# Optimization experiments

Measured on AMD Instinct MI355X. Metric: run time of the kernel, lower is better.

## Reference

```python
import jax, jax.numpy as jnp
import numpy as np

C = 128        # channels
NHEADS = 8
B = 16
HW = 128       # image side; must satisfy HW*HW == C**2 for the module's final view


def setup_inputs() -> dict:
    key = jax.random.key(0)
    k0, k1, k2, k3, k4 = jax.random.split(key, 5)
    x = jax.random.normal(k0, (B, C, HW, HW), jnp.float32)
    w_qkv = jax.random.normal(k1, (3 * C, C), jnp.float32) * 0.02  # 1x1 conv == dense over channel dim
    b_qkv = jax.random.normal(k2, (3 * C,), jnp.float32) * 0.02
    w_out = jax.random.normal(k3, (C, C), jnp.float32) * 0.02
    b_out = jax.random.normal(k4, (C,), jnp.float32) * 0.02
    return {"x": x, "w_qkv": w_qkv, "b_qkv": b_qkv, "w_out": w_out, "b_out": b_out}


def reference(x, w_qkv, b_qkv, w_out, b_out):
    Bx, Cx, Hs, Ws = x.shape
    d = Cx // NHEADS
    N = Hs * Ws  # flattened spatial tokens
    # QKV 1x1 conv (bias=True)
    qkv = jnp.einsum('oc,bchw->bohw', w_qkv, x) + b_qkv[None, :, None, None]
    q, k, v = jnp.split(qkv, 3, axis=1)          # each (B, C, H, W)
    q = q.reshape(Bx, NHEADS, d, N)
    k = k.reshape(Bx, NHEADS, d, N)
    v = v.reshape(Bx, NHEADS, d, N)
    # scaled dot-product attention over the head-channel dim (d x d scores)
    scores = jnp.einsum('bhdn,bhen->bhde', q, k) / jnp.sqrt(jnp.float32(Cx))
    attn = jax.nn.softmax(scores, axis=-1)
    out = jnp.einsum('bhde,bhen->bhdn', attn, v)  # (B, H, d, N)
    side = N // Cx  # module reshapes to (B, C, N//C, N//C); valid since N == C^2
    out = out.reshape(Bx, Cx, side, side)
    # output 1x1 conv
    return jnp.einsum('oc,bchw->bohw', w_out, out) + b_out[None, :, None, None]
```

## Files before the change

kernel.cpp:

```cpp
#include <hip/hip_runtime.h>
#include <math.h>

#define BB 16
#define CC 128
#define NN 16384
#define NHEADS 8
#define HD 16
#define SCALE 0.08838834764831843f

typedef __attribute__((ext_vector_type(8))) short short8;
typedef __attribute__((ext_vector_type(4))) unsigned short ushort4v;
typedef __attribute__((ext_vector_type(16))) float f32x16;

#define CVT(comp, hh, ll)                                                    \
    {                                                                        \
        unsigned int u = __float_as_uint(comp);                              \
        hh = (unsigned short)(u >> 16);                                      \
        float lf = (comp) - __uint_as_float(u & 0xffff0000u);                \
        ll = (unsigned short)(__float_as_uint(lf) >> 16);                    \
    }

__global__ __launch_bounds__(512, 4) void k1_gram(const float* __restrict__ x,
                                                  float* __restrict__ pG,
                                                  float* __restrict__ pS,
                                                  int CH) {
    const int chunk = blockIdx.x;
    const int b = blockIdx.y;
    const int tid = threadIdx.x;
    const int w = tid >> 6;
    const int l = tid & 63;
    const int lr = l & 31, lh = l >> 5;
    const int ch0 = tid >> 4;
    const int t4 = tid & 15;
    const int NCB = NN / CH;
    const int NSTAGE = NCB >> 6;

    __shared__ __align__(16) unsigned short lds[2][2][128 * 64];

    const float* xg = x + (size_t)b * CC * NN + (size_t)chunk * NCB;

    const int bi = w >> 1;
    const int bj0 = (w & 1) * 2;

    f32x16 a0, a1;
#pragma unroll
    for (int r = 0; r < 16; ++r) { a0[r] = 0.0f; a1[r] = 0.0f; }

    float csum[4] = {0.0f, 0.0f, 0.0f, 0.0f};
    float4 ld[4];

    auto LOAD = [&](int s) {
#pragma unroll
        for (int k = 0; k < 4; ++k)
            ld[k] = *(const float4*)(xg + (size_t)(ch0 + 32 * k) * NN + s * 64 + t4 * 4);
    };

    auto CVW = [&](int buf) {
#pragma unroll
        for (int k = 0; k < 4; ++k) {
            float4 v = ld[k];
            csum[k] += v.x + v.y + v.z + v.w;
            const int ch = ch0 + 32 * k;
            const int idx = ((ch << 6) + (t4 << 2)) ^ ((ch & 7) << 3);
            unsigned short h0, h1, h2, h3, l0, l1, l2, l3;
            CVT(v.x, h0, l0)
            CVT(v.y, h1, l1)
            CVT(v.z, h2, l2)
            CVT(v.w, h3, l3)
            ushort4v hv = {h0, h1, h2, h3};
            ushort4v lv = {l0, l1, l2, l3};
            *(ushort4v*)&lds[buf][0][idx] = hv;
            *(ushort4v*)&lds[buf][1][idx] = lv;
        }
    };

    LOAD(0);
    CVW(0);
    __syncthreads();

    const int chA = bi * 32 + lr;
    const int chB0 = bj0 * 32 + lr;
    const int chB1 = chB0 + 32;
    const int swz = (lr & 7) << 3;

    for (int s = 0; s < NSTAGE; ++s) {
        const int bsel = s & 1;
        if (s + 1 < NSTAGE) LOAD(s + 1);

#pragma unroll
        for (int ks = 0; ks < 4; ++ks) {
            const int tok = ks * 16 + 8 * lh;
            const int idxA = ((chA << 6) + tok) ^ swz;
            const int idxB0 = ((chB0 << 6) + tok) ^ swz;
            const int idxB1 = ((chB1 << 6) + tok) ^ swz;
            short8 ah = *(const short8*)&lds[bsel][0][idxA];
            short8 al = *(const short8*)&lds[bsel][1][idxA];
            short8 b0h = *(const short8*)&lds[bsel][0][idxB0];
            short8 b0l = *(const short8*)&lds[bsel][1][idxB0];
            short8 b1h = *(const short8*)&lds[bsel][0][idxB1];
            short8 b1l = *(const short8*)&lds[bsel][1][idxB1];
            a0 = __builtin_amdgcn_mfma_f32_32x32x16_bf16(ah, b0h, a0, 0, 0, 0);
            a0 = __builtin_amdgcn_mfma_f32_32x32x16_bf16(ah, b0l, a0, 0, 0, 0);
            a0 = __builtin_amdgcn_mfma_f32_32x32x16_bf16(al, b0h, a0, 0, 0, 0);
            a1 = __builtin_amdgcn_mfma_f32_32x32x16_bf16(ah, b1h, a1, 0, 0, 0);
            a1 = __builtin_amdgcn_mfma_f32_32x32x16_bf16(ah, b1l, a1, 0, 0, 0);
            a1 = __builtin_amdgcn_mfma_f32_32x32x16_bf16(al, b1h, a1, 0, 0, 0);
        }

        if (s + 1 < NSTAGE) CVW((s + 1) & 1);
        __syncthreads();
    }

    float* scr = (float*)&lds[0][0][0];
#pragma unroll
    for (int k = 0; k < 4; ++k) scr[(ch0 + 32 * k) * 16 + t4] = csum[k];
    __syncthreads();
    if (tid < 128) {
        float s2 = 0.0f;
#pragma unroll
        for (int i = 0; i < 16; ++i) s2 += scr[tid * 16 + i];
        pS[(size_t)(b * CH + chunk) * 128 + tid] = s2;
    }

    float* outp = pG + (size_t)(b * CH + chunk) * 16384;
#pragma unroll
    for (int r = 0; r < 16; ++r) {
        outp[(2 * w) * 1024 + r * 64 + l] = a0[r];
        outp[(2 * w + 1) * 1024 + r * 64 + l] = a1[r];
    }
}

__global__ __launch_bounds__(256) void k1_reduce(const float* __restrict__ pG,
                                                 const float* __restrict__ pS,
                                                 float* __restrict__ G,
                                                 float* __restrict__ sB,
                                                 int CH) {
    const int sg = blockIdx.x;
    const int b = blockIdx.y;
    const int tid = threadIdx.x;

    if (sg < 64) {
        const int e = sg * 256 + tid;
        const int t = e >> 10;
        const int rl = e & 1023;
        float sum = 0.0f;
        const float* p = pG + (size_t)b * CH * 16384 + e;
        for (int ch = 0; ch < CH; ++ch) sum += p[(size_t)ch * 16384];

        const int bi = t >> 2, bj = t & 3;
        const int reg = rl >> 6, lane = rl & 63;
        const int col = bj * 32 + (lane & 31);
        const int row = bi * 32 + (reg & 3) + 8 * (reg >> 2) + 4 * (lane >> 5);
        G[((size_t)b << 14) + row * CC + col] = sum;
    } else {
        if (tid < 128) {
            float s2 = 0.0f;
            for (int ch = 0; ch < CH; ++ch) s2 += pS[(size_t)(b * CH + ch) * 128 + tid];
            sB[b * CC + tid] = s2;
        }
    }
}

__global__ __launch_bounds__(256) void k2a_attn(const float* __restrict__ G,
                                                const float* __restrict__ sB,
                                                const float* __restrict__ w_qkv,
                                                const float* __restrict__ b_qkv,
                                                float* __restrict__ attn,
                                                float* __restrict__ cpre) {
    const int h = blockIdx.x;
    const int b = blockIdx.y;
    const int tid = threadIdx.x;

    __shared__ float Gs[CC * CC];
    __shared__ float wq_s[HD][132], wk_s[HD][132], Tq[HD][132];
    __shared__ float qs[HD], ks[HD], bqv[HD], bkv[HD], bvv[HD];
    __shared__ float sc[HD][HD + 1];

    {
        const float4* Gv = (const float4*)(G + ((size_t)b << 14));
        float4* Gsv = (float4*)Gs;
#pragma unroll
        for (int i = 0; i < 16; ++i) Gsv[tid + 256 * i] = Gv[tid + 256 * i];
    }
    for (int idx = tid; idx < HD * CC; idx += 256) {
        int r = idx >> 7, c = idx & 127;
        wq_s[r][c] = w_qkv[(h * HD + r) * CC + c];
        wk_s[r][c] = w_qkv[(CC + h * HD + r) * CC + c];
    }
    if (tid < HD) {
        bqv[tid] = b_qkv[h * HD + tid];
        bkv[tid] = b_qkv[CC + h * HD + tid];
        bvv[tid] = b_qkv[2 * CC + h * HD + tid];
    }
    __syncthreads();

    if (tid < 32) {
        int i = tid & 15;
        bool isK = tid >= 16;
        float sum = 0.0f;
        for (int c = 0; c < CC; ++c)
            sum += (isK ? wk_s[i][c] : wq_s[i][c]) * sB[b * CC + c];
        if (isK) ks[i] = sum; else qs[i] = sum;
    }

    {
        const int c2 = tid & 127;
        const int dh = tid >> 7;
        float t[8];
#pragma unroll
        for (int j = 0; j < 8; ++j) t[j] = 0.0f;
        for (int c1 = 0; c1 < CC; ++c1) {
            float g = Gs[c1 * CC + c2];
#pragma unroll
            for (int j = 0; j < 8; ++j) t[j] += wq_s[dh * 8 + j][c1] * g;
        }
        __syncthreads();
#pragma unroll
        for (int j = 0; j < 8; ++j) Tq[dh * 8 + j][c2] = t[j];
    }
    __syncthreads();

    {
        const int dd = tid >> 4, e = tid & 15;
        float sum = 0.0f;
        for (int c2 = 0; c2 < CC; ++c2) sum += Tq[dd][c2] * wk_s[e][c2];
        sum += qs[dd] * bkv[e] + bqv[dd] * ks[e] + (float)NN * bqv[dd] * bkv[e];
        sc[dd][e] = sum * SCALE;
    }
    __syncthreads();

    if (tid < HD) {
        const int dd = tid;
        float mx = -1e30f;
#pragma unroll
        for (int e = 0; e < HD; ++e) mx = fmaxf(mx, sc[dd][e]);
        float ex[HD];
        float den = 0.0f;
#pragma unroll
        for (int e = 0; e < HD; ++e) { ex[e] = __expf(sc[dd][e] - mx); den += ex[e]; }
        float inv = 1.0f / den;
        float cp = 0.0f;
#pragma unroll
        for (int e = 0; e < HD; ++e) {
            float a = ex[e] * inv;
            attn[((size_t)b * NHEADS + h) * HD * HD + dd * HD + e] = a;
            cp += a * bvv[e];
        }
        cpre[b * CC + h * HD + dd] = cp;
    }
}

__global__ __launch_bounds__(256) void k2b_M(const float* __restrict__ attn,
                                             const float* __restrict__ cpre,
                                             const float* __restrict__ w_qkv,
                                             const float* __restrict__ w_out,
                                             const float* __restrict__ b_out,
                                             unsigned short* __restrict__ Mh,
                                             unsigned short* __restrict__ Ml,
                                             float* __restrict__ cvec) {
    const int og = blockIdx.x;
    const int b = blockIdx.y;
    const int tid = threadIdx.x;

    __shared__ float Ph[HD][132];
    __shared__ float Vs[HD][132];
    __shared__ float wo_s[32][129];
    __shared__ float attn_s[CC][HD];
    __shared__ float cpre_s[CC];

    for (int idx = tid; idx < CC * HD; idx += 256)
        attn_s[idx >> 4][idx & 15] = attn[(size_t)b * CC * HD + idx];
    for (int idx = tid; idx < 32 * CC; idx += 256)
        wo_s[idx >> 7][idx & 127] = w_out[(og * 32 + (idx >> 7)) * CC + (idx & 127)];
    if (tid < CC) cpre_s[tid] = cpre[b * CC + tid];
    __syncthreads();

    const int c = tid & 127;
    const int oh = tid >> 7;
    float m[16];
#pragma unroll
    for (int j = 0; j < 16; ++j) m[j] = 0.0f;

    for (int hh = 0; hh < NHEADS; ++hh) {
        for (int idx = tid; idx < HD * CC; idx += 256)
            Vs[idx >> 7][idx & 127] = w_qkv[(2 * CC + hh * HD + (idx >> 7)) * CC + (idx & 127)];
        __syncthreads();
        for (int idx = tid; idx < HD * CC; idx += 256) {
            int dd = idx >> 7, cc = idx & 127;
            float s = 0.0f;
#pragma unroll
            for (int e = 0; e < HD; ++e)
                s += attn_s[hh * HD + dd][e] * Vs[e][cc];
            Ph[dd][cc] = s;
        }
        __syncthreads();
#pragma unroll
        for (int dd = 0; dd < HD; ++dd) {
            float p = Ph[dd][c];
#pragma unroll
            for (int j = 0; j < 16; ++j)
                m[j] += wo_s[oh * 16 + j][hh * HD + dd] * p;
        }
        __syncthreads();
    }

#pragma unroll
    for (int j = 0; j < 16; ++j) {
        const int o = og * 32 + oh * 16 + j;
        unsigned short hh2, ll2;
        CVT(m[j], hh2, ll2)
        Mh[((size_t)b << 14) + o * CC + c] = hh2;
        Ml[((size_t)b << 14) + o * CC + c] = ll2;
    }

    if (tid < 32) {
        float s = 0.0f;
        for (int r = 0; r < CC; ++r) s += wo_s[tid][r] * cpre_s[r];
        cvec[b * CC + og * 32 + tid] = s + b_out[og * 32 + tid];
    }
}

__global__ __launch_bounds__(256, 4) void k3_out(const float* __restrict__ x,
                                                 const unsigned short* __restrict__ Mh,
                                                 const unsigned short* __restrict__ Ml,
                                                 const float* __restrict__ cvec,
                                                 float* __restrict__ y) {
    const int chunk = blockIdx.x;
    const int b = blockIdx.y;
    const int tid = threadIdx.x;
    const int w = tid >> 6;
    const int lane = tid & 63;

    __shared__ __align__(16) unsigned short xs[2][2][64 * 128];

    const float* xb = x + (size_t)b * CC * NN + (size_t)chunk * 256;

    short8 Ah[8], Al[8];
    {
        const size_t mbase = ((size_t)b << 14) + (size_t)(32 * w + (lane & 31)) * CC;
#pragma unroll
        for (int ks = 0; ks < 8; ++ks) {
            const size_t off = mbase + 16 * ks + 8 * (lane >> 5);
            Ah[ks] = *(const short8*)&Mh[off];
            Al[ks] = *(const short8*)&Ml[off];
        }
    }

    float cvv[16];
#pragma unroll
    for (int r = 0; r < 16; ++r)
        cvv[r] = cvec[b * CC + 32 * w + (r & 3) + 8 * (r >> 2) + 4 * (lane >> 5)];

    float ldv[4][4];

    auto LOADH = [&](int s, int hf) {
#pragma unroll
        for (int k = 0; k < 4; ++k) {
            const int c0 = w * 4 + (4 * hf + k) * 16;
#pragma unroll
            for (int i = 0; i < 4; ++i)
                ldv[k][i] = xb[(size_t)(c0 + i) * NN + s * 64 + lane];
        }
    };

    auto CVWH = [&](int buf, int hf) {
#pragma unroll
        for (int k = 0; k < 4; ++k) {
            const int c0 = w * 4 + (4 * hf + k) * 16;
            const int idx = lane * 128 + (c0 ^ ((lane & 7) << 3));
            ushort4v hv, lv;
#pragma unroll
            for (int i = 0; i < 4; ++i) {
                unsigned short hh, ll;
                CVT(ldv[k][i], hh, ll)
                hv[i] = hh;
                lv[i] = ll;
            }
            *(ushort4v*)&xs[buf][0][idx] = hv;
            *(ushort4v*)&xs[buf][1][idx] = lv;
        }
    };

    LOADH(0, 0); CVWH(0, 0);
    LOADH(0, 1); CVWH(0, 1);
    __syncthreads();

    float* yb = y + (size_t)b * CC * NN + (size_t)chunk * 256;
    const int nl0 = lane & 31;
    const int cx0 = (nl0 & 7) << 3;
    const int nl1 = 32 + nl0;

    for (int s = 0; s < 4; ++s) {
        const int bsel = s & 1;
        f32x16 a0, a1;
#pragma unroll
        for (int r = 0; r < 16; ++r) { a0[r] = 0.0f; a1[r] = 0.0f; }

        if (s < 3) LOADH(s + 1, 0);

#pragma unroll
        for (int ks = 0; ks < 8; ++ks) {
            const int idx = nl0 * 128 + ((16 * ks + 8 * (lane >> 5)) ^ cx0);
            short8 bh = *(const short8*)&xs[bsel][0][idx];
            short8 bl = *(const short8*)&xs[bsel][1][idx];
            a0 = __builtin_amdgcn_mfma_f32_32x32x16_bf16(Ah[ks], bh, a0, 0, 0, 0);
            a0 = __builtin_amdgcn_mfma_f32_32x32x16_bf16(Ah[ks], bl, a0, 0, 0, 0);
            a0 = __builtin_amdgcn_mfma_f32_32x32x16_bf16(Al[ks], bh, a0, 0, 0, 0);
        }

        if (s < 3) { CVWH(bsel ^ 1, 0); LOADH(s + 1, 1); }

#pragma unroll
        for (int ks = 0; ks < 8; ++ks) {
            const int idx = nl1 * 128 + ((16 * ks + 8 * (lane >> 5)) ^ cx0);
            short8 bh = *(const short8*)&xs[bsel][0][idx];
            short8 bl = *(const short8*)&xs[bsel][1][idx];
            a1 = __builtin_amdgcn_mfma_f32_32x32x16_bf16(Ah[ks], bh, a1, 0, 0, 0);
            a1 = __builtin_amdgcn_mfma_f32_32x32x16_bf16(Ah[ks], bl, a1, 0, 0, 0);
            a1 = __builtin_amdgcn_mfma_f32_32x32x16_bf16(Al[ks], bh, a1, 0, 0, 0);
        }

        if (s < 3) CVWH(bsel ^ 1, 1);

#pragma unroll
        for (int r = 0; r < 16; ++r) {
            const int o = 32 * w + (r & 3) + 8 * (r >> 2) + 4 * (lane >> 5);
            yb[(size_t)o * NN + s * 64 + nl0] = a0[r] + cvv[r];
            yb[(size_t)o * NN + s * 64 + nl1] = a1[r] + cvv[r];
        }
        __syncthreads();
    }
}

extern "C" void kernel_launch(void* const* d_in, const int* in_sizes, int n_in,
                              void* d_out, int out_size, void* d_ws, size_t ws_size,
                              hipStream_t stream) {
    const float* x     = (const float*)d_in[0];
    const float* w_qkv = (const float*)d_in[1];
    const float* b_qkv = (const float*)d_in[2];
    const float* w_out = (const float*)d_in[3];
    const float* b_out = (const float*)d_in[4];
    float* y = (float*)d_out;

    const size_t szG = (size_t)BB * CC * CC;
    const size_t szS = (size_t)BB * CC;
    const size_t szAttn = (size_t)BB * NHEADS * HD * HD;
    const size_t tail = szG + szS + szAttn + szS + szG + szS;

    int CH = 32;
    while (CH > 1 &&
           ((size_t)CH * BB * 16384 + (size_t)CH * BB * CC + tail) * sizeof(float) > ws_size)
        CH >>= 1;

    float* pG   = (float*)d_ws;
    float* pS   = pG + (size_t)CH * BB * 16384;
    float* G    = pS + (size_t)CH * BB * CC;
    float* sB   = G + szG;
    float* attn = sB + szS;
    float* cpre = attn + szAttn;
    float* Mslab = cpre + szS;
    float* cvec = Mslab + szG;

    unsigned short* Mh = (unsigned short*)Mslab;
    unsigned short* Ml = Mh + (size_t)BB * CC * CC;

    k1_gram<<<dim3(CH, BB), 512, 0, stream>>>(x, pG, pS, CH);
    k1_reduce<<<dim3(65, BB), 256, 0, stream>>>(pG, pS, G, sB, CH);
    k2a_attn<<<dim3(NHEADS, BB), 256, 0, stream>>>(G, sB, w_qkv, b_qkv, attn, cpre);
    k2b_M<<<dim3(4, BB), 256, 0, stream>>>(attn, cpre, w_qkv, w_out, b_out, Mh, Ml, cvec);
    k3_out<<<dim3(64, BB), 256, 0, stream>>>(x, Mh, Ml, cvec, y);
}
```

Before: 348.0 us.

## Shrink LDS tiles and restructure Gram and output kernels for higher occupancy

The Gram kernel drops to 256 threads with 32-token stages and a single LDS buffer, and each wave now computes four 32x32 output tiles. The chunk count doubles to 64. The output kernel uses 32-token stages with a single-buffered LDS tile and reads the bias from shared memory. Both kernels raise wave priority around their MFMA loops. The goal is lower LDS footprint and more resident blocks for this memory-bound pipeline, at the cost of an extra barrier per stage, less load/compute overlap, and a larger partial-Gram workspace to reduce.

```diff
diff --git a/kernel.cpp b/kernel.cpp
--- a/kernel.cpp
+++ b/kernel.cpp
@@ -20,7 +20,7 @@
         ll = (unsigned short)(__float_as_uint(lf) >> 16);                    \
     }
 
-__global__ __launch_bounds__(512, 4) void k1_gram(const float* __restrict__ x,
+__global__ __launch_bounds__(256, 4) void k1_gram(const float* __restrict__ x,
                                                   float* __restrict__ pG,
                                                   float* __restrict__ pS,
                                                   int CH) {
@@ -30,104 +30,109 @@
     const int w = tid >> 6;
     const int l = tid & 63;
     const int lr = l & 31, lh = l >> 5;
-    const int ch0 = tid >> 4;
-    const int t4 = tid & 15;
+    const int ch0 = tid >> 3;
+    const int t4 = tid & 7;
     const int NCB = NN / CH;
-    const int NSTAGE = NCB >> 6;
-
-    __shared__ __align__(16) unsigned short lds[2][2][128 * 64];
+    const int NSTAGE = NCB >> 5;
+
+    __shared__ __align__(16) unsigned short lds[2][64 * 64];
+    __shared__ float scr[128 * 8];
 
     const float* xg = x + (size_t)b * CC * NN + (size_t)chunk * NCB;
 
-    const int bi = w >> 1;
-    const int bj0 = (w & 1) * 2;
-
-    f32x16 a0, a1;
-#pragma unroll
-    for (int r = 0; r < 16; ++r) { a0[r] = 0.0f; a1[r] = 0.0f; }
+    f32x16 acc[4];
+#pragma unroll
+    for (int t = 0; t < 4; ++t)
+#pragma unroll
+        for (int r = 0; r < 16; ++r) acc[t][r] = 0.0f;
 
     float csum[4] = {0.0f, 0.0f, 0.0f, 0.0f};
     float4 ld[4];
+    ushort4v hv[4], lv[4];
 
     auto LOAD = [&](int s) {
 #pragma unroll
         for (int k = 0; k < 4; ++k)
-            ld[k] = *(const float4*)(xg + (size_t)(ch0 + 32 * k) * NN + s * 64 + t4 * 4);
-    };
-
-    auto CVW = [&](int buf) {
+            ld[k] = *(const float4*)(xg + (size_t)(ch0 + 32 * k) * NN + s * 32 + t4 * 4);
+    };
+
+    auto CVTALL = [&]() {
 #pragma unroll
         for (int k = 0; k < 4; ++k) {
             float4 v = ld[k];
             csum[k] += v.x + v.y + v.z + v.w;
-            const int ch = ch0 + 32 * k;
-            const int idx = ((ch << 6) + (t4 << 2)) ^ ((ch & 7) << 3);
             unsigned short h0, h1, h2, h3, l0, l1, l2, l3;
             CVT(v.x, h0, l0)
             CVT(v.y, h1, l1)
             CVT(v.z, h2, l2)
             CVT(v.w, h3, l3)
-            ushort4v hv = {h0, h1, h2, h3};
-            ushort4v lv = {l0, l1, l2, l3};
-            *(ushort4v*)&lds[buf][0][idx] = hv;
-            *(ushort4v*)&lds[buf][1][idx] = lv;
+            hv[k] = ushort4v{h0, h1, h2, h3};
+            lv[k] = ushort4v{l0, l1, l2, l3};
+        }
+    };
+
+    auto WR = [&]() {
+#pragma unroll
+        for (int k = 0; k < 4; ++k) {
+            const int ch = ch0 + 32 * k;
+            const int col = ((ch >> 6) * 32 + t4 * 4) ^ ((ch & 7) << 3);
+            const int idx = (ch & 63) * 64 + col;
+            *(ushort4v*)&lds[0][idx] = hv[k];
+            *(ushort4v*)&lds[1][idx] = lv[k];
         }
     };
 
     LOAD(0);
-    CVW(0);
-    __syncthreads();
-
-    const int chA = bi * 32 + lr;
-    const int chB0 = bj0 * 32 + lr;
-    const int chB1 = chB0 + 32;
-    const int swz = (lr & 7) << 3;
+    CVTALL();
+    WR();
+    __syncthreads();
 
     for (int s = 0; s < NSTAGE; ++s) {
-        const int bsel = s & 1;
         if (s + 1 < NSTAGE) LOAD(s + 1);
 
-#pragma unroll
-        for (int ks = 0; ks < 4; ++ks) {
-            const int tok = ks * 16 + 8 * lh;
-            const int idxA = ((chA << 6) + tok) ^ swz;
-            const int idxB0 = ((chB0 << 6) + tok) ^ swz;
-            const int idxB1 = ((chB1 << 6) + tok) ^ swz;
-            short8 ah = *(const short8*)&lds[bsel][0][idxA];
-            short8 al = *(const short8*)&lds[bsel][1][idxA];
-            short8 b0h = *(const short8*)&lds[bsel][0][idxB0];
-            short8 b0l = *(const short8*)&lds[bsel][1][idxB0];
-            short8 b1h = *(const short8*)&lds[bsel][0][idxB1];
-            short8 b1l = *(const short8*)&lds[bsel][1][idxB1];
-            a0 = __builtin_amdgcn_mfma_f32_32x32x16_bf16(ah, b0h, a0, 0, 0, 0);
-            a0 = __builtin_amdgcn_mfma_f32_32x32x16_bf16(ah, b0l, a0, 0, 0, 0);
-            a0 = __builtin_amdgcn_mfma_f32_32x32x16_bf16(al, b0h, a0, 0, 0, 0);
-            a1 = __builtin_amdgcn_mfma_f32_32x32x16_bf16(ah, b1h, a1, 0, 0, 0);
-            a1 = __builtin_amdgcn_mfma_f32_32x32x16_bf16(ah, b1l, a1, 0, 0, 0);
-            a1 = __builtin_amdgcn_mfma_f32_32x32x16_bf16(al, b1h, a1, 0, 0, 0);
-        }
-
-        if (s + 1 < NSTAGE) CVW((s + 1) & 1);
-        __syncthreads();
-    }
-
-    float* scr = (float*)&lds[0][0][0];
-#pragma unroll
-    for (int k = 0; k < 4; ++k) scr[(ch0 + 32 * k) * 16 + t4] = csum[k];
+        __builtin_amdgcn_s_setprio(1);
+#pragma unroll
+        for (int ks = 0; ks < 2; ++ks) {
+            const int tb = ks * 16 + 8 * lh;
+            const int chA = 32 * w + lr;
+            const int idxA = (chA & 63) * 64 + ((((chA >> 6) * 32) + tb) ^ ((chA & 7) << 3));
+            short8 ah = *(const short8*)&lds[0][idxA];
+            short8 al = *(const short8*)&lds[1][idxA];
+#pragma unroll
+            for (int bj = 0; bj < 4; ++bj) {
+                const int chB = 32 * bj + lr;
+                const int idxB = (chB & 63) * 64 + ((((chB >> 6) * 32) + tb) ^ ((chB & 7) << 3));
+                short8 bh = *(const short8*)&lds[0][idxB];
+                short8 bl = *(const short8*)&lds[1][idxB];
+                acc[bj] = __builtin_amdgcn_mfma_f32_32x32x16_bf16(ah, bh, acc[bj], 0, 0, 0);
+                acc[bj] = __builtin_amdgcn_mfma_f32_32x32x16_bf16(ah, bl, acc[bj], 0, 0, 0);
+                acc[bj] = __builtin_amdgcn_mfma_f32_32x32x16_bf16(al, bh, acc[bj], 0, 0, 0);
+            }
+        }
+        __builtin_amdgcn_s_setprio(0);
+
+        if (s + 1 < NSTAGE) CVTALL();
+        __syncthreads();
+        if (s + 1 < NSTAGE) WR();
+        __syncthreads();
+    }
+
+#pragma unroll
+    for (int k = 0; k < 4; ++k) scr[(ch0 + 32 * k) * 8 + t4] = csum[k];
     __syncthreads();
     if (tid < 128) {
         float s2 = 0.0f;
 #pragma unroll
-        for (int i = 0; i < 16; ++i) s2 += scr[tid * 16 + i];
+        for (int i = 0; i < 8; ++i) s2 += scr[tid * 8 + i];
         pS[(size_t)(b * CH + chunk) * 128 + tid] = s2;
     }
 
     float* outp = pG + (size_t)(b * CH + chunk) * 16384;
 #pragma unroll
-    for (int r = 0; r < 16; ++r) {
-        outp[(2 * w) * 1024 + r * 64 + l] = a0[r];
-        outp[(2 * w + 1) * 1024 + r * 64 + l] = a1[r];
-    }
+    for (int bj = 0; bj < 4; ++bj)
+#pragma unroll
+        for (int r = 0; r < 16; ++r)
+            outp[(4 * w + bj) * 1024 + r * 64 + l] = acc[bj][r];
 }
 
 __global__ __launch_bounds__(256) void k1_reduce(const float* __restrict__ pG,
@@ -330,10 +335,15 @@
     const int tid = threadIdx.x;
     const int w = tid >> 6;
     const int lane = tid & 63;
-
-    __shared__ __align__(16) unsigned short xs[2][2][64 * 128];
+    const int st = tid & 31;
+    const int sc0 = (tid >> 5) * 16;
+
+    __shared__ __align__(16) unsigned short xs[2][32 * 128];
+    __shared__ float csl[CC];
 
     const float* xb = x + (size_t)b * CC * NN + (size_t)chunk * 256;
+
+    if (tid < CC) csl[tid] = cvec[b * CC + tid];
 
     short8 Ah[8], Al[8];
     {
@@ -346,88 +356,77 @@
         }
     }
 
-    float cvv[16];
-#pragma unroll
-    for (int r = 0; r < 16; ++r)
-        cvv[r] = cvec[b * CC + 32 * w + (r & 3) + 8 * (r >> 2) + 4 * (lane >> 5)];
-
-    float ldv[4][4];
-
-    auto LOADH = [&](int s, int hf) {
-#pragma unroll
-        for (int k = 0; k < 4; ++k) {
-            const int c0 = w * 4 + (4 * hf + k) * 16;
-#pragma unroll
-            for (int i = 0; i < 4; ++i)
-                ldv[k][i] = xb[(size_t)(c0 + i) * NN + s * 64 + lane];
-        }
-    };
-
-    auto CVWH = [&](int buf, int hf) {
-#pragma unroll
-        for (int k = 0; k < 4; ++k) {
-            const int c0 = w * 4 + (4 * hf + k) * 16;
-            const int idx = lane * 128 + (c0 ^ ((lane & 7) << 3));
-            ushort4v hv, lv;
-#pragma unroll
-            for (int i = 0; i < 4; ++i) {
-                unsigned short hh, ll;
-                CVT(ldv[k][i], hh, ll)
-                hv[i] = hh;
-                lv[i] = ll;
-            }
-            *(ushort4v*)&xs[buf][0][idx] = hv;
-            *(ushort4v*)&xs[buf][1][idx] = lv;
-        }
-    };
-
-    LOADH(0, 0); CVWH(0, 0);
-    LOADH(0, 1); CVWH(0, 1);
+    float ldv[16];
+    ushort4v hv[4], lv[4];
+
+    auto LOAD = [&](int s) {
+#pragma unroll
+        for (int i = 0; i < 16; ++i)
+            ldv[i] = xb[(size_t)(sc0 + i) * NN + s * 32 + st];
+    };
+
+    auto CVTALL = [&]() {
+#pragma unroll
+        for (int g = 0; g < 4; ++g) {
+            unsigned short h0, h1, h2, h3, l0, l1, l2, l3;
+            CVT(ldv[4 * g + 0], h0, l0)
+            CVT(ldv[4 * g + 1], h1, l1)
+            CVT(ldv[4 * g + 2], h2, l2)
+            CVT(ldv[4 * g + 3], h3, l3)
+            hv[g] = ushort4v{h0, h1, h2, h3};
+            lv[g] = ushort4v{l0, l1, l2, l3};
+        }
+    };
+
+    auto WR = [&]() {
+        const int v = (st & 7) << 3;
+        const int rowb = st * 128;
+#pragma unroll
+        for (int g = 0; g < 4; ++g) {
+            const int idx = rowb + ((sc0 + 4 * g) ^ v);
+            *(ushort4v*)&xs[0][idx] = hv[g];
+            *(ushort4v*)&xs[1][idx] = lv[g];
+        }
+    };
+
+    LOAD(0);
+    CVTALL();
+    WR();
     __syncthreads();
 
     float* yb = y + (size_t)b * CC * NN + (size_t)chunk * 256;
-    const int nl0 = lane & 31;
-    const int cx0 = (nl0 & 7) << 3;
-    const int nl1 = 32 + nl0;
-
-    for (int s = 0; s < 4; ++s) {
-        const int bsel = s & 1;
-        f32x16 a0, a1;
-#pragma unroll
-        for (int r = 0; r < 16; ++r) { a0[r] = 0.0f; a1[r] = 0.0f; }
-
-        if (s < 3) LOADH(s + 1, 0);
-
+    const int nl = lane & 31;
+    const int cx = (nl & 7) << 3;
+    const int rowb = nl * 128;
+
+    for (int s = 0; s < 8; ++s) {
+        if (s + 1 < 8) LOAD(s + 1);
+
+        f32x16 a0;
+#pragma unroll
+        for (int r = 0; r < 16; ++r) a0[r] = 0.0f;
+
+        __builtin_amdgcn_s_setprio(1);
 #pragma unroll
         for (int ks = 0; ks < 8; ++ks) {
-            const int idx = nl0 * 128 + ((16 * ks + 8 * (lane >> 5)) ^ cx0);
-            short8 bh = *(const short8*)&xs[bsel][0][idx];
-            short8 bl = *(const short8*)&xs[bsel][1][idx];
+            const int idx = rowb + ((16 * ks + 8 * (lane >> 5)) ^ cx);
+            short8 bh = *(const short8*)&xs[0][idx];
+            short8 bl = *(const short8*)&xs[1][idx];
             a0 = __builtin_amdgcn_mfma_f32_32x32x16_bf16(Ah[ks], bh, a0, 0, 0, 0);
             a0 = __builtin_amdgcn_mfma_f32_32x32x16_bf16(Ah[ks], bl, a0, 0, 0, 0);
             a0 = __builtin_amdgcn_mfma_f32_32x32x16_bf16(Al[ks], bh, a0, 0, 0, 0);
         }
-
-        if (s < 3) { CVWH(bsel ^ 1, 0); LOADH(s + 1, 1); }
-
-#pragma unroll
-        for (int ks = 0; ks < 8; ++ks) {
-            const int idx = nl1 * 128 + ((16 * ks + 8 * (lane >> 5)) ^ cx0);
-            short8 bh = *(const short8*)&xs[bsel][0][idx];
-            short8 bl = *(const short8*)&xs[bsel][1][idx];
-            a1 = __builtin_amdgcn_mfma_f32_32x32x16_bf16(Ah[ks], bh, a1, 0, 0, 0);
-            a1 = __builtin_amdgcn_mfma_f32_32x32x16_bf16(Ah[ks], bl, a1, 0, 0, 0);
-            a1 = __builtin_amdgcn_mfma_f32_32x32x16_bf16(Al[ks], bh, a1, 0, 0, 0);
-        }
-
-        if (s < 3) CVWH(bsel ^ 1, 1);
+        __builtin_amdgcn_s_setprio(0);
 
 #pragma unroll
         for (int r = 0; r < 16; ++r) {
             const int o = 32 * w + (r & 3) + 8 * (r >> 2) + 4 * (lane >> 5);
-            yb[(size_t)o * NN + s * 64 + nl0] = a0[r] + cvv[r];
-            yb[(size_t)o * NN + s * 64 + nl1] = a1[r] + cvv[r];
-        }
+            yb[(size_t)o * NN + s * 32 + nl] = a0[r] + csl[o];
+        }
+
+        if (s + 1 < 8) CVTALL();
+        __syncthreads();
+        if (s + 1 < 8) WR();
         __syncthreads();
     }
 }
@@ -447,7 +446,7 @@
     const size_t szAttn = (size_t)BB * NHEADS * HD * HD;
     const size_t tail = szG + szS + szAttn + szS + szG + szS;
 
-    int CH = 32;
+    int CH = 64;
     while (CH > 1 &&
            ((size_t)CH * BB * 16384 + (size_t)CH * BB * CC + tail) * sizeof(float) > ws_size)
         CH >>= 1;
@@ -464,7 +463,7 @@
     unsigned short* Mh = (unsigned short*)Mslab;
     unsigned short* Ml = Mh + (size_t)BB * CC * CC;
 
-    k1_gram<<<dim3(CH, BB), 512, 0, stream>>>(x, pG, pS, CH);
+    k1_gram<<<dim3(CH, BB), 256, 0, stream>>>(x, pG, pS, CH);
     k1_reduce<<<dim3(65, BB), 256, 0, stream>>>(pG, pS, G, sB, CH);
     k2a_attn<<<dim3(NHEADS, BB), 256, 0, stream>>>(G, sB, w_qkv, b_qkv, attn, cpre);
     k2b_M<<<dim3(4, BB), 256, 0, stream>>>(attn, cpre, w_qkv, w_out, b_out, Mh, Ml, cvec);
```

Measured after the change: 390.3 us. 12.1% more time.
